# Performance work log

Hardware: AMD Instinct MI355X
Metric: run time of the kernel (lower is better)

## Reference

```python
import jax, jax.numpy as jnp
import numpy as np

B, T, N = 128, 64, 9
F_IN = 10
D_ENC = 128
HID = 256
H = 4
C = HID // H
EPS = 1e-5


def _build_edges(b, t):
    # chain adjacency + self loops (as in build_graph), then PyG GATv2Conv
    # remove_self_loops before re-adding mean-filled self loops at runtime.
    A = np.zeros((N, N), dtype=bool)
    i = np.arange(N - 1)
    A[i, i + 1] = True
    A[i + 1, i] = True
    A |= np.eye(N, dtype=bool)
    se = np.argwhere(A).T                       # [2, 25]
    e0 = se.shape[1]
    spatial = np.tile(se, (1, t)) + (np.repeat(np.arange(t), e0) * N)[None, :]
    s = np.arange(N * (t - 1))
    temporal = np.stack([s, s + N])             # forward-in-time edges
    single = np.concatenate([spatial, temporal], axis=1)
    eg = single.shape[1]
    ei = np.tile(single, (1, b)) + (np.repeat(np.arange(b), eg) * (t * N))[None, :]
    ei = ei[:, ei[0] != ei[1]]                  # remove_self_loops
    return jnp.asarray(ei[0]), jnp.asarray(ei[1])


def _forward(node_feats, enc_W, enc_b, layers):
    num_nodes = B * T * N
    types = np.array([0] * 7 + [1, 2])
    onehot = np.eye(3, dtype=np.float32)[types]
    dist = np.abs(np.arange(N) - 7).astype(np.float32)  # chain dist to eef (node 7)
    static = jnp.asarray(np.concatenate([onehot, dist[:, None]], axis=1))  # [N,4]
    feats = jnp.concatenate(
        [node_feats, jnp.broadcast_to(static, (B, T, N, 4))], axis=-1)
    # per-node-type encoders (all same dims -> batched einsum)
    x = (jnp.einsum('btnf,ndf->btnd', feats, enc_W) + enc_b).reshape(num_nodes, D_ENC)
    pos = node_feats[..., :3].reshape(num_nodes, 3)
    src, dst = _build_edges(B, T)
    eattr = pos[dst] - pos[src]
    loops = jnp.arange(num_nodes)
    fill = jnp.broadcast_to(eattr.mean(axis=0), (num_nodes, 3))  # fill_value='mean'
    src = jnp.concatenate([src, loops])
    dst = jnp.concatenate([dst, loops])
    eattr = jnp.concatenate([eattr, fill], axis=0)

    for (lW, lb, rW, rb, att, eW, sW, bias, g, b) in layers:
        xl = (x @ lW.T + lb).reshape(num_nodes, H, C)   # source transform
        xr = (x @ rW.T + rb).reshape(num_nodes, H, C)   # target transform
        em = (eattr @ eW.T).reshape(-1, H, C)
        m = jax.nn.leaky_relu(xl[src] + xr[dst] + em, 0.2)
        logit = jnp.einsum('ehc,hc->eh', m, att)        # [E,H]
        lmax = jax.ops.segment_max(logit, dst, num_segments=num_nodes)
        expv = jnp.exp(logit - lmax[dst])
        denom = jax.ops.segment_sum(expv, dst, num_segments=num_nodes)
        w = expv / denom[dst]                           # segment softmax over dst
        out = jax.ops.segment_sum(xl[src] * w[:, :, None], dst,
                                  num_segments=num_nodes)
        x = out.reshape(num_nodes, HID) + x @ sW.T + bias  # residual + bias
        mu = x.mean(-1, keepdims=True)
        var = ((x - mu) ** 2).mean(-1, keepdims=True)
        x = (x - mu) / jnp.sqrt(var + EPS) * g + b      # LayerNorm
        x = x * jax.nn.sigmoid(x)                       # SiLU
    return x.reshape(B, T * N, HID).mean(axis=1)        # global mean pool


def setup_inputs():
    key = jax.random.key(0)
    ks = iter(jax.random.split(key, 64))
    d = {"node_feats": jax.random.normal(next(ks), (B, T, N, F_IN), jnp.float32)}
    d["enc_W"] = jax.random.normal(next(ks), (N, D_ENC, F_IN + 4), jnp.float32) * 0.1
    d["enc_b"] = jnp.zeros((N, D_ENC), jnp.float32)
    dims = [D_ENC, HID, HID]
    for i in range(3):
        din = dims[i]
        d[f"l{i}_lW"] = jax.random.normal(next(ks), (HID, din), jnp.float32) * 0.05
        d[f"l{i}_lb"] = jnp.zeros((HID,), jnp.float32)
        d[f"l{i}_rW"] = jax.random.normal(next(ks), (HID, din), jnp.float32) * 0.05
        d[f"l{i}_rb"] = jnp.zeros((HID,), jnp.float32)
        d[f"l{i}_att"] = jax.random.normal(next(ks), (H, C), jnp.float32) * 0.1
        d[f"l{i}_eW"] = jax.random.normal(next(ks), (HID, 3), jnp.float32) * 0.1
        d[f"l{i}_sW"] = jax.random.normal(next(ks), (HID, din), jnp.float32) * 0.05
        d[f"l{i}_bias"] = jnp.zeros((HID,), jnp.float32)
        d[f"l{i}_g"] = jnp.ones((HID,), jnp.float32)
        d[f"l{i}_b"] = jnp.zeros((HID,), jnp.float32)
    return d


def reference(node_feats, enc_W, enc_b,
              l0_lW, l0_lb, l0_rW, l0_rb, l0_att, l0_eW, l0_sW, l0_bias, l0_g, l0_b,
              l1_lW, l1_lb, l1_rW, l1_rb, l1_att, l1_eW, l1_sW, l1_bias, l1_g, l1_b,
              l2_lW, l2_lb, l2_rW, l2_rb, l2_att, l2_eW, l2_sW, l2_bias, l2_g, l2_b):
    layers = [
        (l0_lW, l0_lb, l0_rW, l0_rb, l0_att, l0_eW, l0_sW, l0_bias, l0_g, l0_b),
        (l1_lW, l1_lb, l1_rW, l1_rb, l1_att, l1_eW, l1_sW, l1_bias, l1_g, l1_b),
        (l2_lW, l2_lb, l2_rW, l2_rb, l2_att, l2_eW, l2_sW, l2_bias, l2_g, l2_b),
    ]
    return _forward(node_feats, enc_W, enc_b, layers)
```

## Files before the change

kernel.cpp:

```cpp
#include <hip/hip_runtime.h>
#include <hip/hip_bf16.h>
#include <math.h>

#define NODES 73728
#define BB    128
#define TT    64
#define NN    9
#define LDX   256
#define E_REAL 203648.0f
#define NARR  33

typedef _Float16 half8 __attribute__((ext_vector_type(8)));
typedef _Float16 half4 __attribute__((ext_vector_type(4)));
typedef float f32x4 __attribute__((ext_vector_type(4)));

__device__ __forceinline__ float bfdec(unsigned short u) {
  return __uint_as_float(((unsigned)u) << 16);
}
__device__ __forceinline__ unsigned short f2h(float x) {
  _Float16 h = (_Float16)x;
  return __builtin_bit_cast(unsigned short, h);
}

#if __has_builtin(__builtin_amdgcn_fdot2)
#define DOT2(a, b, c) __builtin_amdgcn_fdot2((a), (b), (c), false)
#else
#define DOT2(a, b, c) ((c) + (float)(a)[0] * (float)(b)[0] + (float)(a)[1] * (float)(b)[1])
#endif
#define D2(v, k) __builtin_shufflevector((v), (v), 2 * (k), 2 * (k) + 1)

#define MFMA16(a, b, c) __builtin_amdgcn_mfma_f32_16x16x32_f16((a), (b), (c), 0, 0, 0)
#define SB0() __builtin_amdgcn_sched_barrier(0)

__device__ __forceinline__ void gl_lds16(const _Float16* g, _Float16* l) {
  __builtin_amdgcn_global_load_lds(
      (const __attribute__((address_space(1))) void*)g,
      (__attribute__((address_space(3))) void*)l, 16, 0, 0);
}

__global__ __launch_bounds__(256) void detect_kernel(const unsigned short* __restrict__ raw,
                                                     float* __restrict__ flag) {
  __shared__ float sm[256];
  float mx = 0.f;
  for (int i = threadIdx.x; i < 2048; i += 256) mx = fmaxf(mx, fabsf(bfdec(raw[2 * i])));
  sm[threadIdx.x] = mx;
  __syncthreads();
  for (int s = 128; s > 0; s >>= 1) {
    if (threadIdx.x < s) sm[threadIdx.x] = fmaxf(sm[threadIdx.x], sm[threadIdx.x + s]);
    __syncthreads();
  }
  if (threadIdx.x == 0) flag[0] = (sm[0] > 1000.f) ? 1.f : 0.f;
}

struct CvtArgs { const void* src[NARR]; int size[NARR]; int off[NARR]; };

__global__ __launch_bounds__(256) void convert_kernel(CvtArgs a, const float* __restrict__ flag,
                                                      float* __restrict__ dst,
                                                      _Float16* __restrict__ dsth) {
  int i = blockIdx.y;
  int sz = a.size[i];
  bool isf32 = flag[0] > 0.5f;
  const float* sf = (const float*)a.src[i];
  const unsigned short* sh = (const unsigned short*)a.src[i];
  float* d = dst + a.off[i];
  _Float16* dh = dsth + a.off[i];
  for (int j = blockIdx.x * 256 + threadIdx.x; j < sz; j += gridDim.x * 256) {
    float v = isf32 ? sf[j] : bfdec(sh[j]);
    d[j] = v;
    dh[j] = (_Float16)v;
  }
}

__global__ __launch_bounds__(256) void encoder_kernel(const float* __restrict__ nf,
    const float* __restrict__ encW, const float* __restrict__ encb, _Float16* __restrict__ Xh) {
  int tid = threadIdx.x;
  int v = blockIdx.x * 16 + (tid >> 4);
  int d0 = (tid & 15) << 3;
  int n = v % NN;
  float f[14];
#pragma unroll
  for (int i = 0; i < 10; i++) f[i] = nf[(size_t)v * 10 + i];
  f[10] = (n < 7) ? 1.f : 0.f;
  f[11] = (n == 7) ? 1.f : 0.f;
  f[12] = (n == 8) ? 1.f : 0.f;
  f[13] = fabsf((float)(n - 7));
  half8 o;
#pragma unroll
  for (int j = 0; j < 8; j++) {
    int d = d0 + j;
    const float* w = &encW[((size_t)n * 128 + d) * 14];
    float s = encb[n * 128 + d];
#pragma unroll
    for (int i = 0; i < 14; i++) s = fmaf(f[i], w[i], s);
    o[j] = (_Float16)s;
  }
  *(half8*)&Xh[(size_t)v * LDX + d0] = o;
}

__global__ __launch_bounds__(256) void fill_kernel(const float* __restrict__ nf,
                                                   float* __restrict__ fill) {
  __shared__ float sx[256], sy[256], sz[256];
  int tid = threadIdx.x;
  float ax = 0.f, ay = 0.f, az = 0.f;
  for (int p = tid; p < BB * NN; p += 256) {
    int b = p / NN, n = p - b * NN;
    size_t late  = (((size_t)b * TT + (TT - 1)) * NN + n) * 10;
    size_t early = (((size_t)b * TT) * NN + n) * 10;
    ax += nf[late + 0] - nf[early + 0];
    ay += nf[late + 1] - nf[early + 1];
    az += nf[late + 2] - nf[early + 2];
  }
  sx[tid] = ax; sy[tid] = ay; sz[tid] = az;
  __syncthreads();
  for (int s = 128; s > 0; s >>= 1) {
    if (tid < s) { sx[tid] += sx[tid + s]; sy[tid] += sy[tid + s]; sz[tid] += sz[tid + s]; }
    __syncthreads();
  }
  if (tid == 0) { fill[0] = sx[0] / E_REAL; fill[1] = sy[0] / E_REAL; fill[2] = sz[0] / E_REAL; }
}

template <int K>
__global__ __launch_bounds__(512, 4) void fused3_kernel(
    const _Float16* __restrict__ Xin, _Float16* __restrict__ Xout,
    const _Float16* __restrict__ lW, const float* __restrict__ lb,
    const _Float16* __restrict__ rW, const float* __restrict__ rb,
    const _Float16* __restrict__ sW, const float* __restrict__ sb,
    const float* __restrict__ nf, const float* __restrict__ fill,
    const _Float16* __restrict__ atth, const _Float16* __restrict__ ewh,
    const float* __restrict__ gamma, const float* __restrict__ beta,
    float* pool_out, int do_pool) {
  __shared__ union {
    _Float16 B[8 * 3072];
    struct {
      unsigned short xl[50][264];
      unsigned short epi[32][264];
    } s;
    float pacc[8][256];
  } sh;
  int tid = threadIdx.x;
  int row0 = blockIdx.x * 32;
  const int lane = tid & 63, wv = tid >> 6;
  const int quad = lane >> 4, mrow = lane & 15;
  const int bchunk = (lane & 3) ^ ((lane >> 3) & 3);
  const int rchunk = quad ^ ((mrow >> 1) & 3);
  _Float16* ring = sh.B + wv * 3072;
  const size_t wcol = (size_t)(wv * 32 + (lane >> 2));
  constexpr int NK = K >> 5;
  constexpr size_t wstep = (size_t)16 * K;
  const _Float16* lsrc  = lW + wcol * K + bchunk * 8;
  const _Float16* lsrc2 = lsrc + wstep;
  const _Float16* rsrc  = rW + wcol * K + bchunk * 8;
  const _Float16* rsrc2 = rsrc + wstep;
  const _Float16* ssrc  = sW + wcol * K + bchunk * 8;
  const _Float16* ssrc2 = ssrc + wstep;

  const _Float16* ap[3];
  {
    int gr = (mrow <= 8) ? (row0 - 9 + mrow) : (row0 + 32);
    gr = gr < 0 ? 0 : (gr >= NODES ? NODES - 1 : gr);
    ap[0] = Xin + (size_t)gr * LDX + quad * 8;
    ap[1] = Xin + (size_t)(row0 + mrow) * LDX + quad * 8;
    int r2 = row0 + 16 + mrow; r2 = r2 >= NODES ? NODES - 1 : r2;
    ap[2] = Xin + (size_t)r2 * LDX + quad * 8;
  }

  f32x4 accL[3][2] = {};
  f32x4 accR[2][2] = {};
  f32x4 accS[2][2] = {};
  half8 ab[2][3];

#pragma unroll
  for (int tl = 0; tl < 3; tl++) ab[0][tl] = *(const half8*)ap[tl];
  SB0();
  gl_lds16(lsrc, ring);        gl_lds16(lsrc2, ring + 512);
  gl_lds16(rsrc, ring + 1024); gl_lds16(rsrc2, ring + 1536);
  gl_lds16(ssrc, ring + 2048); gl_lds16(ssrc2, ring + 2560);
  SB0();

#pragma unroll
  for (int t = 0; t < NK; t++) {
    const bool more = (t + 1 < NK);
    const int kn = (t + 1) << 5;
    if (more) {
#pragma unroll
      for (int tl = 0; tl < 3; tl++) ab[(t + 1) & 1][tl] = *(const half8*)(ap[tl] + kn);
    }
    SB0();
    if (more) asm volatile("s_waitcnt vmcnt(7)" ::: "memory");
    else      asm volatile("s_waitcnt vmcnt(4)" ::: "memory");
    SB0();
    {
      half8 b0 = *(const half8*)&ring[(0 * 16 + mrow) * 32 + rchunk * 8];
      half8 b1 = *(const half8*)&ring[(1 * 16 + mrow) * 32 + rchunk * 8];
#pragma unroll
      for (int tl = 0; tl < 3; tl++) {
        accL[tl][0] = MFMA16(ab[t & 1][tl], b0, accL[tl][0]);
        accL[tl][1] = MFMA16(ab[t & 1][tl], b1, accL[tl][1]);
      }
    }
    SB0();
    if (more) { gl_lds16(lsrc + kn, ring); gl_lds16(lsrc2 + kn, ring + 512); }
    SB0();
    if (more) asm volatile("s_waitcnt vmcnt(7)" ::: "memory");
    else      asm volatile("s_waitcnt vmcnt(2)" ::: "memory");
    SB0();
    {
      const _Float16* bb = ring + 1024;
      half8 b0 = *(const half8*)&bb[(0 * 16 + mrow) * 32 + rchunk * 8];
      half8 b1 = *(const half8*)&bb[(1 * 16 + mrow) * 32 + rchunk * 8];
      accR[0][0] = MFMA16(ab[t & 1][1], b0, accR[0][0]);
      accR[1][0] = MFMA16(ab[t & 1][2], b0, accR[1][0]);
      accR[0][1] = MFMA16(ab[t & 1][1], b1, accR[0][1]);
      accR[1][1] = MFMA16(ab[t & 1][2], b1, accR[1][1]);
    }
    SB0();
    if (more) { gl_lds16(rsrc + kn, ring + 1024); gl_lds16(rsrc2 + kn, ring + 1536); }
    SB0();
    if (more) asm volatile("s_waitcnt vmcnt(7)" ::: "memory");
    else      asm volatile("s_waitcnt vmcnt(0)" ::: "memory");
    SB0();
    {
      const _Float16* bb = ring + 2048;
      half8 b0 = *(const half8*)&bb[(0 * 16 + mrow) * 32 + rchunk * 8];
      half8 b1 = *(const half8*)&bb[(1 * 16 + mrow) * 32 + rchunk * 8];
      accS[0][0] = MFMA16(ab[t & 1][1], b0, accS[0][0]);
      accS[1][0] = MFMA16(ab[t & 1][2], b0, accS[1][0]);
      accS[0][1] = MFMA16(ab[t & 1][1], b1, accS[0][1]);
      accS[1][1] = MFMA16(ab[t & 1][2], b1, accS[1][1]);
    }
    SB0();
    if (more) { gl_lds16(ssrc + kn, ring + 2048); gl_lds16(ssrc2 + kn, ring + 2560); }
    SB0();
  }

  __syncthreads();

  {
    int quad_ = lane >> 4, mrow_ = lane & 15;
#pragma unroll
    for (int tl = 0; tl < 3; tl++)
#pragma unroll
      for (int ct = 0; ct < 2; ct++) {
        int col = wv * 32 + ct * 16 + mrow_;
        float bs = lb[col];
#pragma unroll
        for (int r = 0; r < 4; r++) {
          int p = quad_ * 4 + r;
          int xlrow;
          if (tl == 0) xlrow = (p <= 8) ? (p + 7) : ((p == 9) ? 48 : 49);
          else         xlrow = tl * 16 + p;
          sh.s.xl[xlrow][col] = f2h(accL[tl][ct][r] + bs);
        }
      }
#pragma unroll
    for (int rt = 0; rt < 2; rt++)
#pragma unroll
      for (int ct = 0; ct < 2; ct++) {
        int col = wv * 32 + ct * 16 + mrow_;
        float bs = rb[col];
#pragma unroll
        for (int r = 0; r < 4; r++)
          sh.s.epi[rt * 16 + quad_ * 4 + r][col] = f2h(accR[rt][ct][r] + bs);
      }
  }
  __syncthreads();

  {
    int g = lane >> 4;
    int l = lane & 15;
    int ch0 = l << 4;
    half8 att_lo = *(const half8*)&atth[ch0];
    half8 att_hi = *(const half8*)&atth[ch0 + 8];
    half8 ew0l, ew1l, ew2l, ew0h, ew1h, ew2h;
#pragma unroll
    for (int j = 0; j < 8; j++) {
      ew0l[j] = ewh[(ch0 + j) * 3 + 0];      ew0h[j] = ewh[(ch0 + 8 + j) * 3 + 0];
      ew1l[j] = ewh[(ch0 + j) * 3 + 1];      ew1h[j] = ewh[(ch0 + 8 + j) * 3 + 1];
      ew2l[j] = ewh[(ch0 + j) * 3 + 2];      ew2h[j] = ewh[(ch0 + 8 + j) * 3 + 2];
    }
    float f0 = fill[0], f1 = fill[1], f2 = fill[2];
    int r = wv * 4 + g;
    int v = row0 + r;
    int n = v % NN;
    int t = (v / NN) & 63;
    int srcs[4] = { v, (n > 0) ? v - 1 : v, (n < NN - 1) ? v + 1 : v, (t > 0) ? v - NN : v };
    bool valid[4] = { true, n > 0, n < NN - 1, t > 0 };
    float px = nf[(size_t)v * 10 + 0];
    float py = nf[(size_t)v * 10 + 1];
    float pz = nf[(size_t)v * 10 + 2];
    _Float16* erow = (_Float16*)sh.s.epi[r];
    half8 xr_lo = *(const half8*)&erow[ch0];
    half8 xr_hi = *(const half8*)&erow[ch0 + 8];
    half8 xls[4][2];
    float lg[4];
#pragma unroll
    for (int e = 0; e < 4; e++) {
      int s = srcs[e];
      float a0, a1, a2;
      if (e == 0) { a0 = f0; a1 = f1; a2 = f2; }
      else {
        a0 = px - nf[(size_t)s * 10 + 0];
        a1 = py - nf[(size_t)s * 10 + 1];
        a2 = pz - nf[(size_t)s * 10 + 2];
      }
      _Float16 h0 = (_Float16)a0, h1 = (_Float16)a1, h2 = (_Float16)a2;
      const _Float16* xrow = (const _Float16*)sh.s.xl[s - row0 + 16];
      xls[e][0] = *(const half8*)&xrow[ch0];
      xls[e][1] = *(const half8*)&xrow[ch0 + 8];
      half8 mlo = (xr_lo + xls[e][0]) + (ew0l * h0 + ew1l * h1 + ew2l * h2);
      half8 mhi = (xr_hi + xls[e][1]) + (ew0h * h0 + ew1h * h1 + ew2h * h2);
      mlo = __builtin_elementwise_max(mlo, mlo * (_Float16)0.2f);
      mhi = __builtin_elementwise_max(mhi, mhi * (_Float16)0.2f);
      float p = 0.f;
      p = DOT2(D2(mlo, 0), D2(att_lo, 0), p);
      p = DOT2(D2(mlo, 1), D2(att_lo, 1), p);
      p = DOT2(D2(mlo, 2), D2(att_lo, 2), p);
      p = DOT2(D2(mlo, 3), D2(att_lo, 3), p);
      p = DOT2(D2(mhi, 0), D2(att_hi, 0), p);
      p = DOT2(D2(mhi, 1), D2(att_hi, 1), p);
      p = DOT2(D2(mhi, 2), D2(att_hi, 2), p);
      p = DOT2(D2(mhi, 3), D2(att_hi, 3), p);
      p += __shfl_xor(p, 1);
      p += __shfl_xor(p, 2);
      lg[e] = valid[e] ? p : -1e30f;
    }
    float mx = fmaxf(fmaxf(lg[0], lg[1]), fmaxf(lg[2], lg[3]));
    float w0 = __expf(lg[0] - mx), w1 = __expf(lg[1] - mx);
    float w2 = __expf(lg[2] - mx), w3 = __expf(lg[3] - mx);
    float inv = 1.f / (w0 + w1 + w2 + w3);
    float wv4[4] = { w0, w1, w2, w3 };
    half8 agg_lo = { 0, 0, 0, 0, 0, 0, 0, 0 };
    half8 agg_hi = { 0, 0, 0, 0, 0, 0, 0, 0 };
#pragma unroll
    for (int e = 0; e < 4; e++) {
      _Float16 wh = (_Float16)(wv4[e] * inv);
      agg_lo = agg_lo + xls[e][0] * wh;
      agg_hi = agg_hi + xls[e][1] * wh;
    }
    *(half8*)&erow[ch0] = agg_lo;
    *(half8*)&erow[ch0 + 8] = agg_hi;
  }
  __syncthreads();

  {
    int quad_ = lane >> 4, mrow_ = lane & 15;
#pragma unroll
    for (int rt = 0; rt < 2; rt++)
#pragma unroll
      for (int ct = 0; ct < 2; ct++) {
        int col = wv * 32 + ct * 16 + mrow_;
        float bs = sb[col];
#pragma unroll
        for (int rr = 0; rr < 4; rr++) {
          int row = rt * 16 + quad_ * 4 + rr;
          _Float16 ag = *(const _Float16*)&sh.s.epi[row][col];
          sh.s.epi[row][col] = f2h(accS[rt][ct][rr] + bs + (float)ag);
        }
      }
  }
  __syncthreads();

  {
    int cc = lane << 2;
    float gm[4], bt[4];
#pragma unroll
    for (int i = 0; i < 4; i++) { gm[i] = gamma[cc + i]; bt[i] = beta[cc + i]; }
    float psum[4] = { 0.f, 0.f, 0.f, 0.f };
    for (int k = 0; k < 4; k++) {
      int r = wv * 4 + k;
      int v = row0 + r;
      const _Float16* erow = (const _Float16*)sh.s.epi[r];
      half4 x4 = *(const half4*)&erow[cc];
      float xv[4] = { (float)x4[0], (float)x4[1], (float)x4[2], (float)x4[3] };
      float s1 = xv[0] + xv[1] + xv[2] + xv[3];
#pragma unroll
      for (int off = 1; off < 64; off <<= 1) s1 += __shfl_xor(s1, off);
      float mu = s1 * (1.f / 256.f);
      float s2 = 0.f;
#pragma unroll
      for (int i = 0; i < 4; i++) { float d = xv[i] - mu; s2 = fmaf(d, d, s2); }
#pragma unroll
      for (int off = 1; off < 64; off <<= 1) s2 += __shfl_xor(s2, off);
      float rs = rsqrtf(s2 * (1.f / 256.f) + 1e-5f);
      half4 o;
#pragma unroll
      for (int i = 0; i < 4; i++) {
        float y = (xv[i] - mu) * rs * gm[i] + bt[i];
        float z = y * (1.f / (1.f + __expf(-y)));
        o[i] = (_Float16)z;
        psum[i] += z;
      }
      *(half4*)&Xout[(size_t)v * LDX + cc] = o;
    }
    if (do_pool) {
      __syncthreads();
#pragma unroll
      for (int i = 0; i < 4; i++) sh.pacc[wv][cc + i] = psum[i];
      __syncthreads();
      if (wv == 0) {
        int b = row0 / 576;
#pragma unroll
        for (int i = 0; i < 4; i++) {
          float s = 0.f;
#pragma unroll
          for (int w = 0; w < 8; w++) s += sh.pacc[w][cc + i];
          atomicAdd(&pool_out[b * 256 + cc + i], s * (1.f / 576.f));
        }
      }
    }
  }
}

extern "C" void kernel_launch(void* const* d_in, const int* in_sizes, int n_in,
                              void* d_out, int out_size, void* d_ws, size_t ws_size,
                              hipStream_t stream) {
  static const int kSize[NARR] = {
    737280, 16128, 1152,
    32768, 256, 32768, 256, 256, 768, 32768, 256, 256, 256,
    65536, 256, 65536, 256, 256, 768, 65536, 256, 256, 256,
    65536, 256, 65536, 256, 256, 768, 65536, 256, 256, 256
  };
  if (n_in != NARR || out_size != BB * 256) return;
  for (int i = 0; i < NARR; i++) if (in_sizes[i] != kSize[i]) return;

  CvtArgs ca;
  int off = 0;
  for (int i = 0; i < NARR; i++) { ca.src[i] = d_in[i]; ca.size[i] = kSize[i]; ca.off[i] = off; off += kSize[i]; }
  const int PRM_ELEMS = off;

  const size_t OFF_FLAG = 0;
  const size_t OFF_FILL = 16;
  const size_t OFF_PRM  = 256;
  const size_t OFF_PRMH = OFF_PRM + (size_t)PRM_ELEMS * 4;
  const size_t OFF_X0   = OFF_PRMH + (size_t)PRM_ELEMS * 2;
  const size_t OFF_X1   = OFF_X0 + (size_t)NODES * LDX * 2;
  const size_t NEED     = OFF_X1 + (size_t)NODES * LDX * 2;
  if (ws_size < NEED) return;

  char* ws = (char*)d_ws;
  float*     flag = (float*)(ws + OFF_FLAG);
  float*     fill = (float*)(ws + OFF_FILL);
  float*     prm  = (float*)(ws + OFF_PRM);
  _Float16*  prmh = (_Float16*)(ws + OFF_PRMH);
  _Float16*  X0   = (_Float16*)(ws + OFF_X0);
  _Float16*  X1   = (_Float16*)(ws + OFF_X1);

  hipMemsetAsync(d_out, 0, (size_t)out_size * 4, stream);
  detect_kernel<<<1, 256, 0, stream>>>((const unsigned short*)d_in[0], flag);
  convert_kernel<<<dim3(128, NARR), 256, 0, stream>>>(ca, flag, prm, prmh);

  const float* nf   = prm + ca.off[0];
  const float* encW = prm + ca.off[1];
  const float* encb = prm + ca.off[2];

  encoder_kernel<<<NODES / 16, 256, 0, stream>>>(nf, encW, encb, X0);
  fill_kernel<<<1, 256, 0, stream>>>(nf, fill);

  _Float16* Xa = X0;
  _Float16* Xb = X1;
  for (int L = 0; L < 3; L++) {
    const _Float16* lWh = prmh + ca.off[3 + L * 10 + 0];
    const float*    lb  = prm  + ca.off[3 + L * 10 + 1];
    const _Float16* rWh = prmh + ca.off[3 + L * 10 + 2];
    const float*    rb  = prm  + ca.off[3 + L * 10 + 3];
    const _Float16* atth= prmh + ca.off[3 + L * 10 + 4];
    const _Float16* ewhp= prmh + ca.off[3 + L * 10 + 5];
    const _Float16* sWh = prmh + ca.off[3 + L * 10 + 6];
    const float*    sb  = prm  + ca.off[3 + L * 10 + 7];
    const float*    g   = prm  + ca.off[3 + L * 10 + 8];
    const float*    b   = prm  + ca.off[3 + L * 10 + 9];
    if (L == 0)
      fused3_kernel<128><<<NODES / 32, 512, 0, stream>>>(Xa, Xb, lWh, lb, rWh, rb, sWh, sb,
                                                         nf, fill, atth, ewhp, g, b,
                                                         (float*)d_out, 0);
    else
      fused3_kernel<256><<<NODES / 32, 512, 0, stream>>>(Xa, Xb, lWh, lb, rWh, rb, sWh, sb,
                                                         nf, fill, atth, ewhp, g, b,
                                                         (float*)d_out, (L == 2) ? 1 : 0);
    _Float16* tmp = Xa; Xa = Xb; Xb = tmp;
  }
}
```

Measured before the change: 464.8 us.

## Stage activation tile in shared memory once per block instead of per-wave loads

Each of the 8 waves previously loaded the same 48-row activation tile from global memory into registers at every k-step. Now the waves load the whole A tile for all k-steps into LDS once, sharing the work across waves with direct global-to-LDS copies behind a block barrier. The loop then reads A fragments from LDS, and the vmcnt waits are adjusted because per-step A loads no longer count. This cuts redundant global traffic and VGPR pressure, at the cost of more LDS (which could limit occupancy for K=256) and an upfront barrier that removes the overlap of A loads with compute.

```diff
diff --git a/kernel.cpp b/kernel.cpp
--- a/kernel.cpp
+++ b/kernel.cpp
@@ -129,8 +129,12 @@
     const _Float16* __restrict__ atth, const _Float16* __restrict__ ewh,
     const float* __restrict__ gamma, const float* __restrict__ beta,
     float* pool_out, int do_pool) {
+  constexpr int NK = K >> 5;
   __shared__ union {
-    _Float16 B[8 * 3072];
+    struct {
+      _Float16 B[8 * 3072];
+      _Float16 A[3 * NK * 512];
+    } loop;
     struct {
       unsigned short xl[50][264];
       unsigned short epi[32][264];
@@ -143,9 +147,9 @@
   const int quad = lane >> 4, mrow = lane & 15;
   const int bchunk = (lane & 3) ^ ((lane >> 3) & 3);
   const int rchunk = quad ^ ((mrow >> 1) & 3);
-  _Float16* ring = sh.B + wv * 3072;
+  _Float16* ring = sh.loop.B + wv * 3072;
+  _Float16* Ald  = sh.loop.A;
   const size_t wcol = (size_t)(wv * 32 + (lane >> 2));
-  constexpr int NK = K >> 5;
   constexpr size_t wstep = (size_t)16 * K;
   const _Float16* lsrc  = lW + wcol * K + bchunk * 8;
   const _Float16* lsrc2 = lsrc + wstep;
@@ -154,79 +158,81 @@
   const _Float16* ssrc  = sW + wcol * K + bchunk * 8;
   const _Float16* ssrc2 = ssrc + wstep;
 
-  const _Float16* ap[3];
-  {
-    int gr = (mrow <= 8) ? (row0 - 9 + mrow) : (row0 + 32);
-    gr = gr < 0 ? 0 : (gr >= NODES ? NODES - 1 : gr);
-    ap[0] = Xin + (size_t)gr * LDX + quad * 8;
-    ap[1] = Xin + (size_t)(row0 + mrow) * LDX + quad * 8;
-    int r2 = row0 + 16 + mrow; r2 = r2 >= NODES ? NODES - 1 : r2;
-    ap[2] = Xin + (size_t)r2 * LDX + quad * 8;
-  }
-
   f32x4 accL[3][2] = {};
   f32x4 accR[2][2] = {};
   f32x4 accS[2][2] = {};
-  half8 ab[2][3];
-
-#pragma unroll
-  for (int tl = 0; tl < 3; tl++) ab[0][tl] = *(const half8*)ap[tl];
-  SB0();
+
+  {
+    int p = lane >> 2;
+    int gnode = (p <= 8) ? (row0 - 9 + p) : (row0 + 32);
+    gnode = gnode < 0 ? 0 : (gnode >= NODES ? NODES - 1 : gnode);
+    int on0 = row0 + p;
+    int on1 = row0 + 16 + p; on1 = on1 >= NODES ? NODES - 1 : on1;
+#pragma unroll
+    for (int i = 0; i < 3; i++) {
+      int c = wv + i * 8;
+      if (c < 3 * NK) {
+        int t = c / 3, tl = c - t * 3;
+        int node = (tl == 0) ? gnode : ((tl == 1) ? on0 : on1);
+        gl_lds16(Xin + (size_t)node * LDX + t * 32 + bchunk * 8, Ald + c * 512);
+      }
+    }
+  }
   gl_lds16(lsrc, ring);        gl_lds16(lsrc2, ring + 512);
   gl_lds16(rsrc, ring + 1024); gl_lds16(rsrc2, ring + 1536);
   gl_lds16(ssrc, ring + 2048); gl_lds16(ssrc2, ring + 2560);
-  SB0();
+  __syncthreads();
 
 #pragma unroll
   for (int t = 0; t < NK; t++) {
     const bool more = (t + 1 < NK);
     const int kn = (t + 1) << 5;
-    if (more) {
-#pragma unroll
-      for (int tl = 0; tl < 3; tl++) ab[(t + 1) & 1][tl] = *(const half8*)(ap[tl] + kn);
-    }
-    SB0();
-    if (more) asm volatile("s_waitcnt vmcnt(7)" ::: "memory");
-    else      asm volatile("s_waitcnt vmcnt(4)" ::: "memory");
+    const _Float16* abase = Ald + (t * 3) * 512 + mrow * 32 + rchunk * 8;
+    half8 a0 = *(const half8*)abase;
+    half8 a1 = *(const half8*)(abase + 512);
+    half8 a2 = *(const half8*)(abase + 1024);
+    SB0();
+    asm volatile("s_waitcnt vmcnt(4)" ::: "memory");
     SB0();
     {
       half8 b0 = *(const half8*)&ring[(0 * 16 + mrow) * 32 + rchunk * 8];
       half8 b1 = *(const half8*)&ring[(1 * 16 + mrow) * 32 + rchunk * 8];
-#pragma unroll
-      for (int tl = 0; tl < 3; tl++) {
-        accL[tl][0] = MFMA16(ab[t & 1][tl], b0, accL[tl][0]);
-        accL[tl][1] = MFMA16(ab[t & 1][tl], b1, accL[tl][1]);
-      }
+      accL[0][0] = MFMA16(a0, b0, accL[0][0]);
+      accL[0][1] = MFMA16(a0, b1, accL[0][1]);
+      accL[1][0] = MFMA16(a1, b0, accL[1][0]);
+      accL[1][1] = MFMA16(a1, b1, accL[1][1]);
+      accL[2][0] = MFMA16(a2, b0, accL[2][0]);
+      accL[2][1] = MFMA16(a2, b1, accL[2][1]);
     }
     SB0();
     if (more) { gl_lds16(lsrc + kn, ring); gl_lds16(lsrc2 + kn, ring + 512); }
     SB0();
-    if (more) asm volatile("s_waitcnt vmcnt(7)" ::: "memory");
+    if (more) asm volatile("s_waitcnt vmcnt(4)" ::: "memory");
     else      asm volatile("s_waitcnt vmcnt(2)" ::: "memory");
     SB0();
     {
       const _Float16* bb = ring + 1024;
       half8 b0 = *(const half8*)&bb[(0 * 16 + mrow) * 32 + rchunk * 8];
       half8 b1 = *(const half8*)&bb[(1 * 16 + mrow) * 32 + rchunk * 8];
-      accR[0][0] = MFMA16(ab[t & 1][1], b0, accR[0][0]);
-      accR[1][0] = MFMA16(ab[t & 1][2], b0, accR[1][0]);
-      accR[0][1] = MFMA16(ab[t & 1][1], b1, accR[0][1]);
-      accR[1][1] = MFMA16(ab[t & 1][2], b1, accR[1][1]);
+      accR[0][0] = MFMA16(a1, b0, accR[0][0]);
+      accR[1][0] = MFMA16(a2, b0, accR[1][0]);
+      accR[0][1] = MFMA16(a1, b1, accR[0][1]);
+      accR[1][1] = MFMA16(a2, b1, accR[1][1]);
     }
     SB0();
     if (more) { gl_lds16(rsrc + kn, ring + 1024); gl_lds16(rsrc2 + kn, ring + 1536); }
     SB0();
-    if (more) asm volatile("s_waitcnt vmcnt(7)" ::: "memory");
+    if (more) asm volatile("s_waitcnt vmcnt(4)" ::: "memory");
     else      asm volatile("s_waitcnt vmcnt(0)" ::: "memory");
     SB0();
     {
       const _Float16* bb = ring + 2048;
       half8 b0 = *(const half8*)&bb[(0 * 16 + mrow) * 32 + rchunk * 8];
       half8 b1 = *(const half8*)&bb[(1 * 16 + mrow) * 32 + rchunk * 8];
-      accS[0][0] = MFMA16(ab[t & 1][1], b0, accS[0][0]);
-      accS[1][0] = MFMA16(ab[t & 1][2], b0, accS[1][0]);
-      accS[0][1] = MFMA16(ab[t & 1][1], b1, accS[0][1]);
-      accS[1][1] = MFMA16(ab[t & 1][2], b1, accS[1][1]);
+      accS[0][0] = MFMA16(a1, b0, accS[0][0]);
+      accS[1][0] = MFMA16(a2, b0, accS[1][0]);
+      accS[0][1] = MFMA16(a1, b1, accS[0][1]);
+      accS[1][1] = MFMA16(a2, b1, accS[1][1]);
     }
     SB0();
     if (more) { gl_lds16(ssrc + kn, ring + 2048); gl_lds16(ssrc2 + kn, ring + 2560); }
```

After: 425.2 us. 8.5% less time.
